# Kernel optimization log

Measured on AMD Instinct MI355X. Metric: run time of the kernel, lower is better.

## Reference

```python
import jax, jax.numpy as jnp
import numpy as np
import math

D_MODEL = 1024
N_HEADS = 16
D_HEAD = D_MODEL // N_HEADS
B, L, S = 2, 2048, 2048


def setup_inputs() -> dict:
    key = jax.random.key(0)
    ks = jax.random.split(key, 20)
    f32 = jnp.float32
    def lin(k):
        kw, kb = jax.random.split(k)
        W = jax.random.normal(kw, (D_MODEL, D_MODEL), f32) * 0.02
        b = jax.random.normal(kb, (D_MODEL,), f32) * 0.02
        return W, b
    Wq, bq = lin(ks[0]); Wk, bk = lin(ks[1]); Wv, bv = lin(ks[2])
    Wqb, bqb = lin(ks[3]); Wkg, bkg = lin(ks[4]); Wvb, bvb = lin(ks[5])
    Wo, bo = lin(ks[6])
    return {
        "queries": jax.random.normal(ks[7], (B, L, D_MODEL), f32),
        "keys": jax.random.normal(ks[8], (B, S, D_MODEL), f32),
        "values": jax.random.normal(ks[9], (B, S, D_MODEL), f32),
        "attn_mask": jax.random.randint(ks[10], (B, 1, L, S), 0, 2).astype(bool),
        "context": jax.random.normal(ks[11], (B, L, D_MODEL), f32),
        "Wq": Wq, "bq": bq, "Wk": Wk, "bk": bk, "Wv": Wv, "bv": bv,
        "Wqb": Wqb, "bqb": bqb, "Wkg": Wkg, "bkg": bkg, "Wvb": Wvb, "bvb": bvb,
        "Wo": Wo, "bo": bo,
    }


def reference(queries, keys, values, attn_mask, context,
              Wq, bq, Wk, bk, Wv, bv, Wqb, bqb, Wkg, bkg, Wvb, bvb, Wo, bo):
    B_, L_, _ = queries.shape
    S_ = keys.shape[1]
    H, dk = N_HEADS, D_HEAD
    # projections (Linear: x @ W + b), reshaped to [B, T, H, dk]
    Q = (queries @ Wq + bq).reshape(B_, L_, H, dk)
    K = (keys @ Wk + bk).reshape(B_, S_, H, dk)
    V = (values @ Wv + bv).reshape(B_, S_, H, dk)
    # context-based bias / gate
    Q = Q + (context @ Wqb + bqb).reshape(B_, L_, H, dk)
    K = K * jax.nn.sigmoid((context @ Wkg + bkg).reshape(B_, S_, H, dk))
    V = V + (context @ Wvb + bvb).reshape(B_, S_, H, dk)
    # scaled dot-product attention, [B, H, L, S]
    scores = jnp.einsum('blhd,bshd->bhls', Q, K) / math.sqrt(dk)
    scores = jnp.where(attn_mask, jnp.asarray(-1e9, scores.dtype), scores)
    attn_weights = jax.nn.softmax(scores, axis=-1)
    # dropout is identity in eval mode
    out = jnp.einsum('bhls,bshd->blhd', attn_weights, V).reshape(B_, L_, H * dk)
    return (out @ Wo + bo, attn_weights)
```

## Files before the change

kernel.cpp:

```cpp
#include <hip/hip_runtime.h>

typedef __attribute__((ext_vector_type(8))) short  s16x8;
typedef __attribute__((ext_vector_type(8))) unsigned short u16x8;
typedef __attribute__((ext_vector_type(4))) float  f32x4;

#define D_MODEL 1024
#define N_HEADS 16
#define D_HEAD  64
#define BATCH   2
#define SEQ     2048
#define M_TOK   4096

#define OFF_XQ  0u
#define OFF_XK  4194304u
#define OFF_XV  8388608u
#define OFF_XC  12582912u
#define OFF_WT  16777216u
#define OFF_QH  24117248u
#define OFF_KH  28311552u
#define OFF_VH  32505856u
#define OFF_OH  36700160u

__device__ __forceinline__ unsigned short f2bf(float f) {
    unsigned int u = __builtin_bit_cast(unsigned int, f);
    u += 0x7FFFu + ((u >> 16) & 1u);
    return (unsigned short)(u >> 16);
}

__device__ __forceinline__ unsigned int cvtpk(float a, float b) {
    unsigned int r;
    asm("v_cvt_pk_bf16_f32 %0, %1, %2" : "=v"(r) : "v"(a), "v"(b));
    return r;
}

__device__ __forceinline__ void gload16(const void* g, void* l) {
    __builtin_amdgcn_global_load_lds(
        (const __attribute__((address_space(1))) unsigned int*)g,
        (__attribute__((address_space(3))) unsigned int*)l, 16, 0, 0);
}

__device__ __forceinline__ f32x4 mfma16(s16x8 a, s16x8 b, f32x4 c) {
    return __builtin_amdgcn_mfma_f32_16x16x32_bf16(a, b, c, 0, 0, 0);
}

__device__ __forceinline__ f32x4 zero4() {
    f32x4 z; z[0] = 0.f; z[1] = 0.f; z[2] = 0.f; z[3] = 0.f; return z;
}

struct P4 { const float* p[4]; };
struct P7 { const float* p[7]; };

__global__ __launch_bounds__(256) void cvt4(P4 srcs, unsigned short* dst) {
    const int a = blockIdx.y;
    const float* s = srcs.p[a];
    unsigned short* d = dst + ((size_t)a << 22);
    const size_t i = (((size_t)blockIdx.x << 8) + threadIdx.x) << 3;
    const float4 v0 = *(const float4*)(s + i);
    const float4 v1 = *(const float4*)(s + i + 4);
    u16x8 o;
    o[0] = f2bf(v0.x); o[1] = f2bf(v0.y); o[2] = f2bf(v0.z); o[3] = f2bf(v0.w);
    o[4] = f2bf(v1.x); o[5] = f2bf(v1.y); o[6] = f2bf(v1.z); o[7] = f2bf(v1.w);
    *(u16x8*)(d + i) = o;
}

__global__ __launch_bounds__(256) void wtr(P7 srcs, unsigned short* dst) {
    const int z = blockIdx.z;
    const float* W = srcs.p[z];
    unsigned short* Wt = dst + ((size_t)z << 20);
    __shared__ float T[32][33];
    const int t = threadIdx.x;
    const int r = t >> 3, c4 = (t & 7) << 2;
    const int kt = blockIdx.y << 5, nt = blockIdx.x << 5;
    const float4 v = *(const float4*)(W + ((size_t)(kt + r) << 10) + nt + c4);
    T[r][c4] = v.x; T[r][c4 + 1] = v.y; T[r][c4 + 2] = v.z; T[r][c4 + 3] = v.w;
    __syncthreads();
    ushort4 o;
    o.x = f2bf(T[c4 + 0][r]); o.y = f2bf(T[c4 + 1][r]);
    o.z = f2bf(T[c4 + 2][r]); o.w = f2bf(T[c4 + 3][r]);
    *(ushort4*)(Wt + ((size_t)(nt + r) << 10) + kt + c4) = o;
}

__global__ __launch_bounds__(256) void vtr(const unsigned short* __restrict__ Vh,
                                           unsigned short* __restrict__ VhT) {
    __shared__ unsigned short T[64][72];
    const int bh = blockIdx.y, s0 = blockIdx.x << 6;
    const unsigned short* src = Vh + ((size_t)bh * 2048 + s0) * 64;
    unsigned short* dst = VhT + (size_t)bh * 64 * 2048 + s0;
    const int t = threadIdx.x;
    const int r = t >> 3, c0 = (t & 7) << 3;
    #pragma unroll
    for (int it = 0; it < 2; ++it) {
        const int rr = it * 32 + r;
        const u16x8 v = *(const u16x8*)(src + (size_t)rr * 64 + c0);
        #pragma unroll
        for (int i = 0; i < 8; ++i) T[c0 + i][rr] = v[i];
    }
    __syncthreads();
    #pragma unroll
    for (int it = 0; it < 2; ++it) {
        const int rr = it * 32 + r;
        u16x8 o;
        #pragma unroll
        for (int i = 0; i < 8; ++i) o[i] = T[rr][c0 + i];
        *(u16x8*)(dst + (size_t)rr * 2048 + c0) = o;
    }
}

__global__ __launch_bounds__(256) void mpack(const unsigned char* __restrict__ maskp,
                                             unsigned long long* __restrict__ mb) {
    const unsigned int probe = ((const unsigned int*)maskp)[threadIdx.x & 63];
    const bool isInt = __all(probe <= 1u);
    const size_t i = ((size_t)blockIdx.x << 8) + threadIdx.x;
    bool v;
    if (isInt) v = ((const int*)maskp)[i] != 0;
    else       v = maskp[i] != 0;
    const unsigned long long bal = __ballot(v);
    if ((threadIdx.x & 63) == 0) mb[i >> 6] = bal;
}

struct ProjDesc {
    const unsigned short *A0, *A1, *B0, *B1;
    const float *b0, *b1;
    unsigned short* dst;
    float scale;
    int gate;
};
struct ProjArgs { ProjDesc d[3]; };

__global__ __launch_bounds__(256) void proj_all(ProjArgs pa) {
    const ProjDesc P = pa.d[blockIdx.z];
    __shared__ unsigned short Al[2][128 * 32];
    __shared__ unsigned short Bl[2][64 * 32];
    const int tid = threadIdx.x;
    const int wid = tid >> 6, lane = tid & 63;
    const int lo = lane & 15, hi = lane >> 4;
    const int wr = wid >> 1, wc = wid & 1;
    const int m0 = blockIdx.y << 7, n0 = blockIdx.x << 6;

    auto stageT = [&](int t) {
        const int bufi = t & 1;
        const unsigned short* As = (t < 32) ? P.A0 : P.A1;
        const unsigned short* Bs = (t < 32) ? P.B0 : P.B1;
        const int k0 = (t & 31) << 5;
        #pragma unroll
        for (int it = 0; it < 2; ++it) {
            const int c = it * 256 + tid;
            const int r = c >> 2, j = c & 3;
            gload16(As + ((size_t)(m0 + r) << 10) + k0 + j * 8, &Al[bufi][c * 8]);
        }
        const int rb = tid >> 2, jb = tid & 3;
        gload16(Bs + ((size_t)(n0 + rb) << 10) + k0 + jb * 8, &Bl[bufi][tid * 8]);
    };

    f32x4 acc0[4][2], acc1[4][2];
    #pragma unroll
    for (int i = 0; i < 4; ++i)
        #pragma unroll
        for (int j = 0; j < 2; ++j) { acc0[i][j] = zero4(); acc1[i][j] = zero4(); }

    stageT(0);
    for (int t = 0; t < 64; ++t) {
        __syncthreads();
        if (t < 63) stageT(t + 1);
        const int bufi = t & 1;
        s16x8 af[4], bfr[2];
        #pragma unroll
        for (int mi = 0; mi < 4; ++mi)
            af[mi] = *(const s16x8*)&Al[bufi][(wr * 64 + mi * 16 + lo) * 32 + hi * 8];
        #pragma unroll
        for (int ni = 0; ni < 2; ++ni)
            bfr[ni] = *(const s16x8*)&Bl[bufi][(wc * 32 + ni * 16 + lo) * 32 + hi * 8];
        __builtin_amdgcn_s_setprio(1);
        if (t < 32) {
            #pragma unroll
            for (int mi = 0; mi < 4; ++mi)
                #pragma unroll
                for (int ni = 0; ni < 2; ++ni)
                    acc0[mi][ni] = mfma16(af[mi], bfr[ni], acc0[mi][ni]);
        } else {
            #pragma unroll
            for (int mi = 0; mi < 4; ++mi)
                #pragma unroll
                for (int ni = 0; ni < 2; ++ni)
                    acc1[mi][ni] = mfma16(af[mi], bfr[ni], acc1[mi][ni]);
        }
        __builtin_amdgcn_s_setprio(0);
    }

    #pragma unroll
    for (int mi = 0; mi < 4; ++mi)
        #pragma unroll
        for (int ni = 0; ni < 2; ++ni) {
            const int n = n0 + wc * 32 + ni * 16 + lo;
            const float b0 = P.b0[n], b1 = P.b1[n];
            const int h = n >> 6, d = n & 63;
            #pragma unroll
            for (int reg = 0; reg < 4; ++reg) {
                const int m = m0 + wr * 64 + mi * 16 + hi * 4 + reg;
                const int b = m >> 11, t = m & 2047;
                float val;
                if (P.gate) {
                    const float kv = acc0[mi][ni][reg] + b0;
                    const float gv = acc1[mi][ni][reg] + b1;
                    val = kv * (1.0f / (1.0f + __expf(-gv)));
                } else {
                    val = (acc0[mi][ni][reg] + acc1[mi][ni][reg] + b0 + b1) * P.scale;
                }
                P.dst[((size_t)((b * 16 + h) * 2048 + t) << 6) + d] = f2bf(val);
            }
        }
}

__global__ __launch_bounds__(256) void gemm_out(
    const unsigned short* __restrict__ A, const unsigned short* __restrict__ Bt,
    const float* __restrict__ bias, float* __restrict__ out)
{
    __shared__ unsigned short Al[2][128 * 32];
    __shared__ unsigned short Bl[2][64 * 32];
    const int tid = threadIdx.x;
    const int wid = tid >> 6, lane = tid & 63;
    const int lo = lane & 15, hi = lane >> 4;
    const int wr = wid >> 1, wc = wid & 1;
    const int m0 = blockIdx.y << 7, n0 = blockIdx.x << 6;

    auto stageT = [&](int t) {
        const int bufi = t & 1;
        const int k0 = t << 5;
        #pragma unroll
        for (int it = 0; it < 2; ++it) {
            const int c = it * 256 + tid;
            const int r = c >> 2, j = c & 3;
            gload16(A + ((size_t)(m0 + r) << 10) + k0 + j * 8, &Al[bufi][c * 8]);
        }
        const int rb = tid >> 2, jb = tid & 3;
        gload16(Bt + ((size_t)(n0 + rb) << 10) + k0 + jb * 8, &Bl[bufi][tid * 8]);
    };

    f32x4 acc[4][2];
    #pragma unroll
    for (int i = 0; i < 4; ++i)
        #pragma unroll
        for (int j = 0; j < 2; ++j) acc[i][j] = zero4();

    stageT(0);
    for (int t = 0; t < 32; ++t) {
        __syncthreads();
        if (t < 31) stageT(t + 1);
        const int bufi = t & 1;
        s16x8 af[4], bfr[2];
        #pragma unroll
        for (int mi = 0; mi < 4; ++mi)
            af[mi] = *(const s16x8*)&Al[bufi][(wr * 64 + mi * 16 + lo) * 32 + hi * 8];
        #pragma unroll
        for (int ni = 0; ni < 2; ++ni)
            bfr[ni] = *(const s16x8*)&Bl[bufi][(wc * 32 + ni * 16 + lo) * 32 + hi * 8];
        __builtin_amdgcn_s_setprio(1);
        #pragma unroll
        for (int mi = 0; mi < 4; ++mi)
            #pragma unroll
            for (int ni = 0; ni < 2; ++ni)
                acc[mi][ni] = mfma16(af[mi], bfr[ni], acc[mi][ni]);
        __builtin_amdgcn_s_setprio(0);
    }

    #pragma unroll
    for (int mi = 0; mi < 4; ++mi)
        #pragma unroll
        for (int ni = 0; ni < 2; ++ni) {
            const int n = n0 + wc * 32 + ni * 16 + lo;
            const float bb = bias[n];
            #pragma unroll
            for (int reg = 0; reg < 4; ++reg) {
                const int m = m0 + wr * 64 + mi * 16 + hi * 4 + reg;
                out[((size_t)m << 10) + n] = acc[mi][ni][reg] + bb;
            }
        }
}

__global__ __launch_bounds__(256, 4) void attn_fused(
    const unsigned short* __restrict__ Qh, const unsigned short* __restrict__ Kh,
    const unsigned short* __restrict__ VhT, const unsigned long long* __restrict__ mbits,
    float* __restrict__ attnW, unsigned short* __restrict__ Oh)
{
    __shared__ unsigned short Ks[2][4096];
    __shared__ unsigned short Vs[2][4096];
    __shared__ unsigned short Ps[4][1024];

    const int tid = threadIdx.x;
    const int wid = tid >> 6, lane = tid & 63;
    const int lo = lane & 15, hi = lane >> 4;

    const int wg = blockIdx.x;
    const int gid = (wg & 7) * 128 + (wg >> 3);
    const int bh = gid >> 5, lt = gid & 31;
    const int b = bh >> 4, hh = bh & 15;
    const int l0 = lt << 6;

    const unsigned short* Qp = Qh + ((size_t)bh * 2048 + l0) * 64;
    const unsigned short* Kp = Kh + (size_t)bh * 2048 * 64;
    const unsigned short* Vp = VhT + (size_t)bh * 64 * 2048;

    const int q = wid * 16 + lo;
    float* Wrow = attnW + ((size_t)bh * 2048 + l0 + q) * 2048 + hi * 4;
    const unsigned long long* mq = mbits + ((size_t)b * 2048 + l0 + q) * 32;

    s16x8 qf[2];
    {
        const unsigned short* qr = Qp + (size_t)q * 64 + hi * 8;
        qf[0] = *(const s16x8*)qr;
        qf[1] = *(const s16x8*)(qr + 32);
    }

    auto stageK = [&](int st, int bufi) {
        const unsigned short* src = Kp + (size_t)(st << 6) * 64;
        #pragma unroll
        for (int it = 0; it < 2; ++it) {
            const int c = it * 256 + tid;
            const int r = c >> 3, j = c & 7;
            gload16(src + (size_t)r * 64 + ((j ^ (r & 7)) << 3), &Ks[bufi][c * 8]);
        }
    };
    auto stageV = [&](int st, int bufi) {
        const unsigned short* src = Vp + (st << 6);
        #pragma unroll
        for (int it = 0; it < 2; ++it) {
            const int c = it * 256 + tid;
            const int r = c >> 3, j = c & 7;
            gload16(src + (size_t)r * 2048 + ((j ^ (r & 7)) << 3), &Vs[bufi][c * 8]);
        }
    };

    float lsum = 0.f;
    stageK(0, 0);
    __syncthreads();
    for (int st = 0; st < 32; ++st) {
        const int cur = st & 1;
        if (st < 31) stageK(st + 1, cur ^ 1);

        const unsigned long long mrow = mq[st] >> (hi * 4);
        f32x4 sf[4];
        #pragma unroll
        for (int ni = 0; ni < 4; ++ni) sf[ni] = zero4();
        __builtin_amdgcn_s_setprio(1);
        #pragma unroll
        for (int ks = 0; ks < 2; ++ks)
            #pragma unroll
            for (int ni = 0; ni < 4; ++ni) {
                const int rn = ni * 16 + lo;
                const s16x8 kf = *(const s16x8*)&Ks[cur][rn * 64 + (((hi + ks * 4) ^ (rn & 7)) << 3)];
                sf[ni] = mfma16(kf, qf[ks], sf[ni]);
            }
        __builtin_amdgcn_s_setprio(0);
        #pragma unroll
        for (int ni = 0; ni < 4; ++ni)
            #pragma unroll
            for (int reg = 0; reg < 4; ++reg) {
                const unsigned int bit = (unsigned int)(mrow >> (ni * 16 + reg)) & 1u;
                lsum += bit ? 0.f : exp2f(sf[ni][reg]);
            }
        __syncthreads();
    }
    lsum += __shfl_xor(lsum, 16);
    lsum += __shfl_xor(lsum, 32);
    const float il = 1.0f / lsum;

    f32x4 oacc[4];
    #pragma unroll
    for (int nd = 0; nd < 4; ++nd) oacc[nd] = zero4();

    stageK(0, 0);
    stageV(0, 0);
    __syncthreads();
    for (int st = 0; st < 32; ++st) {
        const int cur = st & 1;
        if (st < 31) { stageK(st + 1, cur ^ 1); stageV(st + 1, cur ^ 1); }

        const unsigned long long mrow = mq[st] >> (hi * 4);
        f32x4 sf[4];
        #pragma unroll
        for (int ni = 0; ni < 4; ++ni) sf[ni] = zero4();
        __builtin_amdgcn_s_setprio(1);
        #pragma unroll
        for (int ks = 0; ks < 2; ++ks)
            #pragma unroll
            for (int ni = 0; ni < 4; ++ni) {
                const int rn = ni * 16 + lo;
                const s16x8 kf = *(const s16x8*)&Ks[cur][rn * 64 + (((hi + ks * 4) ^ (rn & 7)) << 3)];
                sf[ni] = mfma16(kf, qf[ks], sf[ni]);
            }
        __builtin_amdgcn_s_setprio(0);

        #pragma unroll
        for (int ni = 0; ni < 4; ++ni) {
            f32x4 wv;
            #pragma unroll
            for (int reg = 0; reg < 4; ++reg) {
                const unsigned int bit = (unsigned int)(mrow >> (ni * 16 + reg)) & 1u;
                const float e = bit ? 0.f : exp2f(sf[ni][reg]);
                wv[reg] = e * il;
            }
            __builtin_nontemporal_store(wv, (f32x4*)(Wrow + (size_t)st * 64 + ni * 16));
            const unsigned int p01 = cvtpk(wv[0], wv[1]);
            const unsigned int p23 = cvtpk(wv[2], wv[3]);
            *(uint2*)((char*)&Ps[wid][0] + lo * 128 + ((ni * 32 + hi * 8) ^ ((lo & 7) << 4))) =
                make_uint2(p01, p23);
        }

        __builtin_amdgcn_s_setprio(1);
        #pragma unroll
        for (int ks = 0; ks < 2; ++ks) {
            const s16x8 pf = *(const s16x8*)((const char*)&Ps[wid][0] +
                lo * 128 + ((ks * 64 + hi * 16) ^ ((lo & 7) << 4)));
            #pragma unroll
            for (int nd = 0; nd < 4; ++nd) {
                const int rv = nd * 16 + lo;
                const s16x8 vf = *(const s16x8*)&Vs[cur][rv * 64 + (((hi + ks * 4) ^ (rv & 7)) << 3)];
                oacc[nd] = mfma16(pf, vf, oacc[nd]);
            }
        }
        __builtin_amdgcn_s_setprio(0);
        __syncthreads();
    }

    #pragma unroll
    for (int nd = 0; nd < 4; ++nd)
        #pragma unroll
        for (int reg = 0; reg < 4; ++reg) {
            const int rl = wid * 16 + hi * 4 + reg;
            const int d = nd * 16 + lo;
            Oh[((size_t)(b * 2048 + l0 + rl) << 10) + hh * 64 + d] = f2bf(oacc[nd][reg]);
        }
}

extern "C" void kernel_launch(void* const* d_in, const int* in_sizes, int n_in,
                              void* d_out, int out_size, void* d_ws, size_t ws_size,
                              hipStream_t stream) {
    const float* queries = (const float*)d_in[0];
    const float* keys    = (const float*)d_in[1];
    const float* values  = (const float*)d_in[2];
    const unsigned char* mask = (const unsigned char*)d_in[3];
    const float* context = (const float*)d_in[4];
    const float* Wq  = (const float*)d_in[5];  const float* bq  = (const float*)d_in[6];
    const float* Wk  = (const float*)d_in[7];  const float* bk  = (const float*)d_in[8];
    const float* Wv  = (const float*)d_in[9];  const float* bv  = (const float*)d_in[10];
    const float* Wqb = (const float*)d_in[11]; const float* bqb = (const float*)d_in[12];
    const float* Wkg = (const float*)d_in[13]; const float* bkg = (const float*)d_in[14];
    const float* Wvb = (const float*)d_in[15]; const float* bvb = (const float*)d_in[16];
    const float* Wo  = (const float*)d_in[17]; const float* bo  = (const float*)d_in[18];

    unsigned short* ws = (unsigned short*)d_ws;
    unsigned short* xq = ws + OFF_XQ;
    unsigned short* xk = ws + OFF_XK;
    unsigned short* xv = ws + OFF_XV;
    unsigned short* xc = ws + OFF_XC;
    unsigned short* wt = ws + OFF_WT;
    unsigned short* Qh = ws + OFF_QH;
    unsigned short* Kh = ws + OFF_KH;
    unsigned short* Vh = ws + OFF_VH;
    unsigned short* Oh = ws + OFF_OH;
    unsigned short* VhT = ws + OFF_XQ;
    unsigned long long* mbits = (unsigned long long*)(ws + OFF_XV);

    float* out0  = (float*)d_out;
    float* attnW = out0 + 4194304;

    P4 acts; acts.p[0] = queries; acts.p[1] = keys; acts.p[2] = values; acts.p[3] = context;
    cvt4<<<dim3(2048, 4), 256, 0, stream>>>(acts, xq);

    P7 wts; wts.p[0] = Wq; wts.p[1] = Wqb; wts.p[2] = Wk; wts.p[3] = Wkg;
    wts.p[4] = Wv; wts.p[5] = Wvb; wts.p[6] = Wo;
    wtr<<<dim3(32, 32, 7), 256, 0, stream>>>(wts, wt);

    ProjArgs pa;
    pa.d[0] = { xq, xc, wt, wt + 1048576u, bq, bqb, Qh, 0.18033688f, 0 };
    pa.d[1] = { xv, xc, wt + 4u * 1048576u, wt + 5u * 1048576u, bv, bvb, Vh, 1.0f, 0 };
    pa.d[2] = { xk, xc, wt + 2u * 1048576u, wt + 3u * 1048576u, bk, bkg, Kh, 1.0f, 1 };
    proj_all<<<dim3(16, 32, 3), 256, 0, stream>>>(pa);

    vtr<<<dim3(32, 32), 256, 0, stream>>>(Vh, VhT);
    mpack<<<dim3(32768), 256, 0, stream>>>(mask, mbits);

    attn_fused<<<dim3(1024), 256, 0, stream>>>(Qh, Kh, VhT, mbits, attnW, Oh);

    gemm_out<<<dim3(16, 32), 256, 0, stream>>>(Oh, wt + 6u * 1048576u, bo, out0);
}
```

Baseline: 372.9 us.

## Deepen K prefetch to quad buffers with explicit vmcnt waits in attention

```diff
diff --git a/kernel.cpp b/kernel.cpp
--- a/kernel.cpp
+++ b/kernel.cpp
@@ -20,6 +20,10 @@
 #define OFF_KH  28311552u
 #define OFF_VH  32505856u
 #define OFF_OH  36700160u
+
+#define WAITV(N) asm volatile("s_waitcnt vmcnt(" #N ")" ::: "memory")
+#define SCHED0() __builtin_amdgcn_sched_barrier(0)
+#define SBAR()   __builtin_amdgcn_s_barrier()
 
 __device__ __forceinline__ unsigned short f2bf(float f) {
     unsigned int u = __builtin_bit_cast(unsigned int, f);
@@ -282,9 +286,7 @@
     const unsigned short* __restrict__ VhT, const unsigned long long* __restrict__ mbits,
     float* __restrict__ attnW, unsigned short* __restrict__ Oh)
 {
-    __shared__ unsigned short Ks[2][4096];
-    __shared__ unsigned short Vs[2][4096];
-    __shared__ unsigned short Ps[4][1024];
+    __shared__ unsigned short SMEM[20480];
 
     const int tid = threadIdx.x;
     const int wid = tid >> 6, lane = tid & 63;
@@ -304,6 +306,8 @@
     float* Wrow = attnW + ((size_t)bh * 2048 + l0 + q) * 2048 + hi * 4;
     const unsigned long long* mq = mbits + ((size_t)b * 2048 + l0 + q) * 32;
 
+    unsigned short* Pw = &SMEM[16384 + (wid << 10)];
+
     s16x8 qf[2];
     {
         const unsigned short* qr = Qp + (size_t)q * 64 + hi * 8;
@@ -311,33 +315,40 @@
         qf[1] = *(const s16x8*)(qr + 32);
     }
 
-    auto stageK = [&](int st, int bufi) {
+    auto kbuf = [&](int i) -> unsigned short* { return &SMEM[i << 12]; };
+
+    auto stageK = [&](int st, int bi) {
         const unsigned short* src = Kp + (size_t)(st << 6) * 64;
+        unsigned short* dstb = kbuf(bi);
         #pragma unroll
         for (int it = 0; it < 2; ++it) {
             const int c = it * 256 + tid;
             const int r = c >> 3, j = c & 7;
-            gload16(src + (size_t)r * 64 + ((j ^ (r & 7)) << 3), &Ks[bufi][c * 8]);
+            gload16(src + (size_t)r * 64 + ((j ^ (r & 7)) << 3), dstb + c * 8);
         }
     };
-    auto stageV = [&](int st, int bufi) {
+    auto stageV = [&](int st, int bi) {
         const unsigned short* src = Vp + (st << 6);
+        unsigned short* dstb = kbuf(bi);
         #pragma unroll
         for (int it = 0; it < 2; ++it) {
             const int c = it * 256 + tid;
             const int r = c >> 3, j = c & 7;
-            gload16(src + (size_t)r * 2048 + ((j ^ (r & 7)) << 3), &Vs[bufi][c * 8]);
+            gload16(src + (size_t)r * 2048 + ((j ^ (r & 7)) << 3), dstb + c * 8);
         }
     };
 
     float lsum = 0.f;
     stageK(0, 0);
-    __syncthreads();
+    stageK(1, 1);
+    unsigned long long mrow = mq[0];
+    WAITV(3); SCHED0();
     for (int st = 0; st < 32; ++st) {
-        const int cur = st & 1;
-        if (st < 31) stageK(st + 1, cur ^ 1);
-
-        const unsigned long long mrow = mq[st] >> (hi * 4);
+        SBAR(); SCHED0();
+        if (st + 2 < 32) stageK(st + 2, (st + 2) & 3);
+        const unsigned long long mnext = (st + 1 < 32) ? mq[st + 1] : 0ull;
+
+        const unsigned short* kb = kbuf(st & 3);
         f32x4 sf[4];
         #pragma unroll
         for (int ni = 0; ni < 4; ++ni) sf[ni] = zero4();
@@ -347,18 +358,23 @@
             #pragma unroll
             for (int ni = 0; ni < 4; ++ni) {
                 const int rn = ni * 16 + lo;
-                const s16x8 kf = *(const s16x8*)&Ks[cur][rn * 64 + (((hi + ks * 4) ^ (rn & 7)) << 3)];
+                const s16x8 kf = *(const s16x8*)&kb[rn * 64 + (((hi + ks * 4) ^ (rn & 7)) << 3)];
                 sf[ni] = mfma16(kf, qf[ks], sf[ni]);
             }
         __builtin_amdgcn_s_setprio(0);
+
+        const unsigned long long mr = mrow >> (hi * 4);
         #pragma unroll
         for (int ni = 0; ni < 4; ++ni)
             #pragma unroll
             for (int reg = 0; reg < 4; ++reg) {
-                const unsigned int bit = (unsigned int)(mrow >> (ni * 16 + reg)) & 1u;
+                const unsigned int bit = (unsigned int)(mr >> (ni * 16 + reg)) & 1u;
                 lsum += bit ? 0.f : exp2f(sf[ni][reg]);
             }
-        __syncthreads();
+        mrow = mnext;
+
+        if (st < 30)      { WAITV(3); SCHED0(); }
+        else if (st == 30){ WAITV(1); SCHED0(); }
     }
     lsum += __shfl_xor(lsum, 16);
     lsum += __shfl_xor(lsum, 32);
@@ -368,14 +384,19 @@
     #pragma unroll
     for (int nd = 0; nd < 4; ++nd) oacc[nd] = zero4();
 
+    __syncthreads();
     stageK(0, 0);
-    stageV(0, 0);
-    __syncthreads();
+    stageV(0, 2);
+    mrow = mq[0];
+    WAITV(0); SCHED0();
     for (int st = 0; st < 32; ++st) {
-        const int cur = st & 1;
-        if (st < 31) { stageK(st + 1, cur ^ 1); stageV(st + 1, cur ^ 1); }
-
-        const unsigned long long mrow = mq[st] >> (hi * 4);
+        SBAR(); SCHED0();
+        if (st + 1 < 32) { stageK(st + 1, (st + 1) & 1); stageV(st + 1, 2 + ((st + 1) & 1)); }
+        const unsigned long long mnext = (st + 1 < 32) ? mq[st + 1] : 0ull;
+
+        const unsigned short* kb = kbuf(st & 1);
+        const unsigned short* vb = kbuf(2 + (st & 1));
+
         f32x4 sf[4];
         #pragma unroll
         for (int ni = 0; ni < 4; ++ni) sf[ni] = zero4();
@@ -385,41 +406,44 @@
             #pragma unroll
             for (int ni = 0; ni < 4; ++ni) {
                 const int rn = ni * 16 + lo;
-                const s16x8 kf = *(const s16x8*)&Ks[cur][rn * 64 + (((hi + ks * 4) ^ (rn & 7)) << 3)];
+                const s16x8 kf = *(const s16x8*)&kb[rn * 64 + (((hi + ks * 4) ^ (rn & 7)) << 3)];
                 sf[ni] = mfma16(kf, qf[ks], sf[ni]);
             }
         __builtin_amdgcn_s_setprio(0);
 
+        const unsigned long long mr = mrow >> (hi * 4);
         #pragma unroll
         for (int ni = 0; ni < 4; ++ni) {
             f32x4 wv;
             #pragma unroll
             for (int reg = 0; reg < 4; ++reg) {
-                const unsigned int bit = (unsigned int)(mrow >> (ni * 16 + reg)) & 1u;
+                const unsigned int bit = (unsigned int)(mr >> (ni * 16 + reg)) & 1u;
                 const float e = bit ? 0.f : exp2f(sf[ni][reg]);
                 wv[reg] = e * il;
             }
             __builtin_nontemporal_store(wv, (f32x4*)(Wrow + (size_t)st * 64 + ni * 16));
             const unsigned int p01 = cvtpk(wv[0], wv[1]);
             const unsigned int p23 = cvtpk(wv[2], wv[3]);
-            *(uint2*)((char*)&Ps[wid][0] + lo * 128 + ((ni * 32 + hi * 8) ^ ((lo & 7) << 4))) =
+            *(uint2*)((char*)Pw + lo * 128 + ((ni * 32 + hi * 8) ^ ((lo & 7) << 4))) =
                 make_uint2(p01, p23);
         }
+        mrow = mnext;
 
         __builtin_amdgcn_s_setprio(1);
         #pragma unroll
         for (int ks = 0; ks < 2; ++ks) {
-            const s16x8 pf = *(const s16x8*)((const char*)&Ps[wid][0] +
+            const s16x8 pf = *(const s16x8*)((const char*)Pw +
                 lo * 128 + ((ks * 64 + hi * 16) ^ ((lo & 7) << 4)));
             #pragma unroll
             for (int nd = 0; nd < 4; ++nd) {
                 const int rv = nd * 16 + lo;
-                const s16x8 vf = *(const s16x8*)&Vs[cur][rv * 64 + (((hi + ks * 4) ^ (rv & 7)) << 3)];
+                const s16x8 vf = *(const s16x8*)&vb[rv * 64 + (((hi + ks * 4) ^ (rv & 7)) << 3)];
                 oacc[nd] = mfma16(pf, vf, oacc[nd]);
             }
         }
         __builtin_amdgcn_s_setprio(0);
-        __syncthreads();
+
+        if (st + 1 < 32) { WAITV(5); SCHED0(); }
     }
 
     #pragma unroll
```

Result: slower. 383.6 us (+2.9%).

## Widen projection tile to 128x128 and compute sigmoid gate mid-loop into packed bf16

Applied to the files above, without the earlier changes.

```diff
diff --git a/kernel.cpp b/kernel.cpp
--- a/kernel.cpp
+++ b/kernel.cpp
@@ -31,6 +31,10 @@
     unsigned int r;
     asm("v_cvt_pk_bf16_f32 %0, %1, %2" : "=v"(r) : "v"(a), "v"(b));
     return r;
+}
+
+__device__ __forceinline__ float bf2f(unsigned int low16) {
+    return __builtin_bit_cast(float, low16 << 16);
 }
 
 __device__ __forceinline__ void gload16(const void* g, void* l) {
@@ -130,69 +134,84 @@
 __global__ __launch_bounds__(256) void proj_all(ProjArgs pa) {
     const ProjDesc P = pa.d[blockIdx.z];
     __shared__ unsigned short Al[2][128 * 32];
-    __shared__ unsigned short Bl[2][64 * 32];
+    __shared__ unsigned short Bl[2][128 * 32];
     const int tid = threadIdx.x;
     const int wid = tid >> 6, lane = tid & 63;
     const int lo = lane & 15, hi = lane >> 4;
     const int wr = wid >> 1, wc = wid & 1;
-    const int m0 = blockIdx.y << 7, n0 = blockIdx.x << 6;
+    const int m0 = blockIdx.y << 7, n0 = blockIdx.x << 7;
 
     auto stageT = [&](int t) {
         const int bufi = t & 1;
-        const unsigned short* As = (t < 32) ? P.A0 : P.A1;
-        const unsigned short* Bs = (t < 32) ? P.B0 : P.B1;
+        const unsigned short *As, *Bs;
+        if (P.gate) { As = (t < 32) ? P.A1 : P.A0; Bs = (t < 32) ? P.B1 : P.B0; }
+        else        { As = (t < 32) ? P.A0 : P.A1; Bs = (t < 32) ? P.B0 : P.B1; }
         const int k0 = (t & 31) << 5;
         #pragma unroll
         for (int it = 0; it < 2; ++it) {
             const int c = it * 256 + tid;
             const int r = c >> 2, j = c & 3;
             gload16(As + ((size_t)(m0 + r) << 10) + k0 + j * 8, &Al[bufi][c * 8]);
-        }
-        const int rb = tid >> 2, jb = tid & 3;
-        gload16(Bs + ((size_t)(n0 + rb) << 10) + k0 + jb * 8, &Bl[bufi][tid * 8]);
+            gload16(Bs + ((size_t)(n0 + r) << 10) + k0 + j * 8, &Bl[bufi][c * 8]);
+        }
     };
 
-    f32x4 acc0[4][2], acc1[4][2];
+    f32x4 acc[4][4];
     #pragma unroll
     for (int i = 0; i < 4; ++i)
         #pragma unroll
-        for (int j = 0; j < 2; ++j) { acc0[i][j] = zero4(); acc1[i][j] = zero4(); }
+        for (int j = 0; j < 4; ++j) acc[i][j] = zero4();
+
+    unsigned int sg[4][8];
 
     stageT(0);
     for (int t = 0; t < 64; ++t) {
         __syncthreads();
         if (t < 63) stageT(t + 1);
+
+        if (P.gate && t == 32) {
+            #pragma unroll
+            for (int mi = 0; mi < 4; ++mi)
+                #pragma unroll
+                for (int ni = 0; ni < 4; ++ni) {
+                    const int n = n0 + wc * 64 + ni * 16 + lo;
+                    const float b1v = P.b1[n];
+                    #pragma unroll
+                    for (int pr = 0; pr < 2; ++pr) {
+                        const float g0 = acc[mi][ni][pr * 2]     + b1v;
+                        const float g1 = acc[mi][ni][pr * 2 + 1] + b1v;
+                        const float s0 = 1.0f / (1.0f + __expf(-g0));
+                        const float s1 = 1.0f / (1.0f + __expf(-g1));
+                        sg[mi][ni * 2 + pr] = cvtpk(s0, s1);
+                    }
+                    acc[mi][ni] = zero4();
+                }
+        }
+
         const int bufi = t & 1;
-        s16x8 af[4], bfr[2];
+        s16x8 af[4], bfr[4];
         #pragma unroll
         for (int mi = 0; mi < 4; ++mi)
             af[mi] = *(const s16x8*)&Al[bufi][(wr * 64 + mi * 16 + lo) * 32 + hi * 8];
         #pragma unroll
-        for (int ni = 0; ni < 2; ++ni)
-            bfr[ni] = *(const s16x8*)&Bl[bufi][(wc * 32 + ni * 16 + lo) * 32 + hi * 8];
+        for (int ni = 0; ni < 4; ++ni)
+            bfr[ni] = *(const s16x8*)&Bl[bufi][(wc * 64 + ni * 16 + lo) * 32 + hi * 8];
         __builtin_amdgcn_s_setprio(1);
-        if (t < 32) {
-            #pragma unroll
-            for (int mi = 0; mi < 4; ++mi)
-                #pragma unroll
-                for (int ni = 0; ni < 2; ++ni)
-                    acc0[mi][ni] = mfma16(af[mi], bfr[ni], acc0[mi][ni]);
-        } else {
-            #pragma unroll
-            for (int mi = 0; mi < 4; ++mi)
-                #pragma unroll
-                for (int ni = 0; ni < 2; ++ni)
-                    acc1[mi][ni] = mfma16(af[mi], bfr[ni], acc1[mi][ni]);
-        }
+        #pragma unroll
+        for (int mi = 0; mi < 4; ++mi)
+            #pragma unroll
+            for (int ni = 0; ni < 4; ++ni)
+                acc[mi][ni] = mfma16(af[mi], bfr[ni], acc[mi][ni]);
         __builtin_amdgcn_s_setprio(0);
     }
 
     #pragma unroll
     for (int mi = 0; mi < 4; ++mi)
         #pragma unroll
-        for (int ni = 0; ni < 2; ++ni) {
-            const int n = n0 + wc * 32 + ni * 16 + lo;
-            const float b0 = P.b0[n], b1 = P.b1[n];
+        for (int ni = 0; ni < 4; ++ni) {
+            const int n = n0 + wc * 64 + ni * 16 + lo;
+            const float b0 = P.b0[n];
+            const float b1 = P.b1[n];
             const int h = n >> 6, d = n & 63;
             #pragma unroll
             for (int reg = 0; reg < 4; ++reg) {
@@ -200,11 +219,11 @@
                 const int b = m >> 11, t = m & 2047;
                 float val;
                 if (P.gate) {
-                    const float kv = acc0[mi][ni][reg] + b0;
-                    const float gv = acc1[mi][ni][reg] + b1;
-                    val = kv * (1.0f / (1.0f + __expf(-gv)));
+                    const unsigned int pk = sg[mi][ni * 2 + (reg >> 1)];
+                    const float sgf = bf2f((reg & 1) ? (pk >> 16) : (pk & 0xFFFFu));
+                    val = (acc[mi][ni][reg] + b0) * sgf;
                 } else {
-                    val = (acc0[mi][ni][reg] + acc1[mi][ni][reg] + b0 + b1) * P.scale;
+                    val = (acc[mi][ni][reg] + b0 + b1) * P.scale;
                 }
                 P.dst[((size_t)((b * 16 + h) * 2048 + t) << 6) + d] = f2bf(val);
             }
@@ -475,7 +494,7 @@
     pa.d[0] = { xq, xc, wt, wt + 1048576u, bq, bqb, Qh, 0.18033688f, 0 };
     pa.d[1] = { xv, xc, wt + 4u * 1048576u, wt + 5u * 1048576u, bv, bvb, Vh, 1.0f, 0 };
     pa.d[2] = { xk, xc, wt + 2u * 1048576u, wt + 3u * 1048576u, bk, bkg, Kh, 1.0f, 1 };
-    proj_all<<<dim3(16, 32, 3), 256, 0, stream>>>(pa);
+    proj_all<<<dim3(8, 32, 3), 256, 0, stream>>>(pa);
 
     vtr<<<dim3(32, 32), 256, 0, stream>>>(Vh, VhT);
     mpack<<<dim3(32768), 256, 0, stream>>>(mask, mbits);
```

Result: slower. 403.4 us (+8.2%).

## Split gate sigmoid into separate GEMM and widen projection tiles to 128x128

Applied to the files above, without the earlier changes.

```diff
diff --git a/kernel.cpp b/kernel.cpp
--- a/kernel.cpp
+++ b/kernel.cpp
@@ -31,6 +31,10 @@
     unsigned int r;
     asm("v_cvt_pk_bf16_f32 %0, %1, %2" : "=v"(r) : "v"(a), "v"(b));
     return r;
+}
+
+__device__ __forceinline__ float bf2f(unsigned short u) {
+    return __builtin_bit_cast(float, (unsigned int)u << 16);
 }
 
 __device__ __forceinline__ void gload16(const void* g, void* l) {
@@ -118,17 +122,10 @@
     if ((threadIdx.x & 63) == 0) mb[i >> 6] = bal;
 }
 
-struct ProjDesc {
-    const unsigned short *A0, *A1, *B0, *B1;
-    const float *b0, *b1;
-    unsigned short* dst;
-    float scale;
-    int gate;
-};
-struct ProjArgs { ProjDesc d[3]; };
-
-__global__ __launch_bounds__(256) void proj_all(ProjArgs pa) {
-    const ProjDesc P = pa.d[blockIdx.z];
+__global__ __launch_bounds__(256) void proj_gate_sig(
+    const unsigned short* __restrict__ A, const unsigned short* __restrict__ Bt,
+    const float* __restrict__ bias, unsigned short* __restrict__ sgT)
+{
     __shared__ unsigned short Al[2][128 * 32];
     __shared__ unsigned short Bl[2][64 * 32];
     const int tid = threadIdx.x;
@@ -139,6 +136,84 @@
 
     auto stageT = [&](int t) {
         const int bufi = t & 1;
+        const int k0 = t << 5;
+        #pragma unroll
+        for (int it = 0; it < 2; ++it) {
+            const int c = it * 256 + tid;
+            const int r = c >> 2, j = c & 3;
+            gload16(A + ((size_t)(m0 + r) << 10) + k0 + j * 8, &Al[bufi][c * 8]);
+        }
+        const int rb = tid >> 2, jb = tid & 3;
+        gload16(Bt + ((size_t)(n0 + rb) << 10) + k0 + jb * 8, &Bl[bufi][tid * 8]);
+    };
+
+    f32x4 acc[4][2];
+    #pragma unroll
+    for (int i = 0; i < 4; ++i)
+        #pragma unroll
+        for (int j = 0; j < 2; ++j) acc[i][j] = zero4();
+
+    stageT(0);
+    for (int t = 0; t < 32; ++t) {
+        __syncthreads();
+        if (t < 31) stageT(t + 1);
+        const int bufi = t & 1;
+        s16x8 af[4], bfr[2];
+        #pragma unroll
+        for (int mi = 0; mi < 4; ++mi)
+            af[mi] = *(const s16x8*)&Al[bufi][(wr * 64 + mi * 16 + lo) * 32 + hi * 8];
+        #pragma unroll
+        for (int ni = 0; ni < 2; ++ni)
+            bfr[ni] = *(const s16x8*)&Bl[bufi][(wc * 32 + ni * 16 + lo) * 32 + hi * 8];
+        __builtin_amdgcn_s_setprio(1);
+        #pragma unroll
+        for (int mi = 0; mi < 4; ++mi)
+            #pragma unroll
+            for (int ni = 0; ni < 2; ++ni)
+                acc[mi][ni] = mfma16(af[mi], bfr[ni], acc[mi][ni]);
+        __builtin_amdgcn_s_setprio(0);
+    }
+
+    #pragma unroll
+    for (int mi = 0; mi < 4; ++mi)
+        #pragma unroll
+        for (int ni = 0; ni < 2; ++ni) {
+            const int n = n0 + wc * 32 + ni * 16 + lo;
+            const float bb = bias[n];
+            const int mb = m0 + wr * 64 + mi * 16 + hi * 4;
+            ushort4 o;
+            unsigned short* op = (unsigned short*)&o;
+            #pragma unroll
+            for (int reg = 0; reg < 4; ++reg) {
+                const float g = acc[mi][ni][reg] + bb;
+                op[reg] = f2bf(1.0f / (1.0f + __expf(-g)));
+            }
+            *(ushort4*)(sgT + (size_t)n * 4096 + mb) = o;
+        }
+}
+
+struct ProjDesc {
+    const unsigned short *A0, *A1, *B0, *B1;
+    const float *b0, *b1;
+    unsigned short* dst;
+    float scale;
+    int gate;
+    int nsteps;
+};
+struct ProjArgs { ProjDesc d[3]; };
+
+__global__ __launch_bounds__(256) void proj_all(ProjArgs pa, const unsigned short* __restrict__ sgT) {
+    const ProjDesc P = pa.d[blockIdx.z];
+    __shared__ unsigned short Al[2][128 * 32];
+    __shared__ unsigned short Bl[2][128 * 32];
+    const int tid = threadIdx.x;
+    const int wid = tid >> 6, lane = tid & 63;
+    const int lo = lane & 15, hi = lane >> 4;
+    const int wr = wid >> 1, wc = wid & 1;
+    const int m0 = blockIdx.y << 7, n0 = blockIdx.x << 7;
+
+    auto stageT = [&](int t) {
+        const int bufi = t & 1;
         const unsigned short* As = (t < 32) ? P.A0 : P.A1;
         const unsigned short* Bs = (t < 32) ? P.B0 : P.B1;
         const int k0 = (t & 31) << 5;
@@ -147,65 +222,57 @@
             const int c = it * 256 + tid;
             const int r = c >> 2, j = c & 3;
             gload16(As + ((size_t)(m0 + r) << 10) + k0 + j * 8, &Al[bufi][c * 8]);
-        }
-        const int rb = tid >> 2, jb = tid & 3;
-        gload16(Bs + ((size_t)(n0 + rb) << 10) + k0 + jb * 8, &Bl[bufi][tid * 8]);
+            gload16(Bs + ((size_t)(n0 + r) << 10) + k0 + j * 8, &Bl[bufi][c * 8]);
+        }
     };
 
-    f32x4 acc0[4][2], acc1[4][2];
+    f32x4 acc[4][4];
     #pragma unroll
     for (int i = 0; i < 4; ++i)
         #pragma unroll
-        for (int j = 0; j < 2; ++j) { acc0[i][j] = zero4(); acc1[i][j] = zero4(); }
-
+        for (int j = 0; j < 4; ++j) acc[i][j] = zero4();
+
+    const int nsteps = P.nsteps;
     stageT(0);
-    for (int t = 0; t < 64; ++t) {
+    for (int t = 0; t < nsteps; ++t) {
         __syncthreads();
-        if (t < 63) stageT(t + 1);
+        if (t + 1 < nsteps) stageT(t + 1);
         const int bufi = t & 1;
-        s16x8 af[4], bfr[2];
+        s16x8 af[4], bfr[4];
         #pragma unroll
         for (int mi = 0; mi < 4; ++mi)
             af[mi] = *(const s16x8*)&Al[bufi][(wr * 64 + mi * 16 + lo) * 32 + hi * 8];
         #pragma unroll
-        for (int ni = 0; ni < 2; ++ni)
-            bfr[ni] = *(const s16x8*)&Bl[bufi][(wc * 32 + ni * 16 + lo) * 32 + hi * 8];
+        for (int ni = 0; ni < 4; ++ni)
+            bfr[ni] = *(const s16x8*)&Bl[bufi][(wc * 64 + ni * 16 + lo) * 32 + hi * 8];
         __builtin_amdgcn_s_setprio(1);
-        if (t < 32) {
-            #pragma unroll
-            for (int mi = 0; mi < 4; ++mi)
-                #pragma unroll
-                for (int ni = 0; ni < 2; ++ni)
-                    acc0[mi][ni] = mfma16(af[mi], bfr[ni], acc0[mi][ni]);
-        } else {
-            #pragma unroll
-            for (int mi = 0; mi < 4; ++mi)
-                #pragma unroll
-                for (int ni = 0; ni < 2; ++ni)
-                    acc1[mi][ni] = mfma16(af[mi], bfr[ni], acc1[mi][ni]);
-        }
+        #pragma unroll
+        for (int mi = 0; mi < 4; ++mi)
+            #pragma unroll
+            for (int ni = 0; ni < 4; ++ni)
+                acc[mi][ni] = mfma16(af[mi], bfr[ni], acc[mi][ni]);
         __builtin_amdgcn_s_setprio(0);
     }
 
     #pragma unroll
     for (int mi = 0; mi < 4; ++mi)
         #pragma unroll
-        for (int ni = 0; ni < 2; ++ni) {
-            const int n = n0 + wc * 32 + ni * 16 + lo;
-            const float b0 = P.b0[n], b1 = P.b1[n];
+        for (int ni = 0; ni < 4; ++ni) {
+            const int n = n0 + wc * 64 + ni * 16 + lo;
+            const float b0 = P.b0[n];
+            const float b1 = P.b1[n];
             const int h = n >> 6, d = n & 63;
+            const int mb = m0 + wr * 64 + mi * 16 + hi * 4;
+            ushort4 sgv;
+            if (P.gate) sgv = *(const ushort4*)(sgT + (size_t)n * 4096 + mb);
+            const unsigned short* sp = (const unsigned short*)&sgv;
             #pragma unroll
             for (int reg = 0; reg < 4; ++reg) {
-                const int m = m0 + wr * 64 + mi * 16 + hi * 4 + reg;
+                const int m = mb + reg;
                 const int b = m >> 11, t = m & 2047;
                 float val;
-                if (P.gate) {
-                    const float kv = acc0[mi][ni][reg] + b0;
-                    const float gv = acc1[mi][ni][reg] + b1;
-                    val = kv * (1.0f / (1.0f + __expf(-gv)));
-                } else {
-                    val = (acc0[mi][ni][reg] + acc1[mi][ni][reg] + b0 + b1) * P.scale;
-                }
+                if (P.gate) val = (acc[mi][ni][reg] + b0) * bf2f(sp[reg]);
+                else        val = (acc[mi][ni][reg] + b0 + b1) * P.scale;
                 P.dst[((size_t)((b * 16 + h) * 2048 + t) << 6) + d] = f2bf(val);
             }
         }
@@ -458,6 +525,7 @@
     unsigned short* Kh = ws + OFF_KH;
     unsigned short* Vh = ws + OFF_VH;
     unsigned short* Oh = ws + OFF_OH;
+    unsigned short* sgT = ws + OFF_OH;
     unsigned short* VhT = ws + OFF_XQ;
     unsigned long long* mbits = (unsigned long long*)(ws + OFF_XV);
 
@@ -471,11 +539,13 @@
     wts.p[4] = Wv; wts.p[5] = Wvb; wts.p[6] = Wo;
     wtr<<<dim3(32, 32, 7), 256, 0, stream>>>(wts, wt);
 
+    proj_gate_sig<<<dim3(16, 32), 256, 0, stream>>>(xc, wt + 3u * 1048576u, bkg, sgT);
+
     ProjArgs pa;
-    pa.d[0] = { xq, xc, wt, wt + 1048576u, bq, bqb, Qh, 0.18033688f, 0 };
-    pa.d[1] = { xv, xc, wt + 4u * 1048576u, wt + 5u * 1048576u, bv, bvb, Vh, 1.0f, 0 };
-    pa.d[2] = { xk, xc, wt + 2u * 1048576u, wt + 3u * 1048576u, bk, bkg, Kh, 1.0f, 1 };
-    proj_all<<<dim3(16, 32, 3), 256, 0, stream>>>(pa);
+    pa.d[0] = { xq, xc, wt, wt + 1048576u, bq, bqb, Qh, 0.18033688f, 0, 64 };
+    pa.d[1] = { xv, xc, wt + 4u * 1048576u, wt + 5u * 1048576u, bv, bvb, Vh, 1.0f, 0, 64 };
+    pa.d[2] = { xk, xk, wt + 2u * 1048576u, wt + 2u * 1048576u, bk, bk, Kh, 1.0f, 1, 32 };
+    proj_all<<<dim3(8, 32, 3), 256, 0, stream>>>(pa, sgT);
 
     vtr<<<dim3(32, 32), 256, 0, stream>>>(Vh, VhT);
     mpack<<<dim3(32768), 256, 0, stream>>>(mask, mbits);
```

Measured after the change: 348.0 us (median of 3 runs). -6.7%, faster.
